# Performance work log

Hardware: AMD Instinct MI355X
Metric: run time of the kernel (lower is better)

## Reference

```python
import jax, jax.numpy as jnp
import numpy as np

N, LAT, H, R, L = 384, 64, 128, 16, 3
CUTOFF = 12.0
COORD_INIT_SCALE = 0.001


def setup_inputs() -> dict:
    key = jax.random.key(0)
    ks = jax.random.split(key, 12)
    def w(k, shape, fan):
        return jax.random.normal(k, shape, jnp.float32) / np.float32(np.sqrt(fan))
    return {
        "z": jax.random.normal(ks[0], (N, LAT), jnp.float32),
        # spread anchors so the radius graph is non-trivially sparse
        "anchor_coords": jax.random.normal(ks[1], (N, 3), jnp.float32) * 10.0,
        "proj_W": w(ks[2], (LAT, H), LAT),
        "proj_b": jnp.zeros((H,), jnp.float32),
        "eW1": w(ks[3], (L, 2 * H + R, H), 2 * H + R),
        "eb1": jnp.zeros((L, H), jnp.float32),
        "eW2": w(ks[4], (L, H, H), H),
        "eb2": jnp.zeros((L, H), jnp.float32),
        "nW1": w(ks[5], (L, 2 * H, H), 2 * H),
        "nb1": jnp.zeros((L, H), jnp.float32),
        "nW2": w(ks[6], (L, H, H), H),
        "nb2": jnp.zeros((L, H), jnp.float32),
        "cW1": w(ks[7], (L, H, H), H),
        "cb1": jnp.zeros((L, H), jnp.float32),
        # coord head scaled by coord_update_init_scale for stable coordinate updates
        "cW2": w(ks[8], (L, H, 1), H) * COORD_INIT_SCALE,
    }


def _rbf(d):
    # Gaussian radial basis expansion over [0, cutoff]
    mu = jnp.linspace(0.0, CUTOFF, R, dtype=d.dtype)            # (R,)
    gamma = jnp.asarray((R / CUTOFF) ** 2, d.dtype)
    return jnp.exp(-gamma * (d[..., None] - mu) ** 2)           # (..., R)


def reference(z, anchor_coords, proj_W, proj_b, eW1, eb1, eW2, eb2,
              nW1, nb1, nW2, nb2, cW1, cb1, cW2):
    silu = jax.nn.silu
    n = z.shape[0]
    h = z @ proj_W + proj_b                                      # (N, H)
    x = anchor_coords - anchor_coords.mean(0, keepdims=True)     # (N, 3)

    idx = jnp.arange(n)
    seq_mask = jnp.abs(idx[:, None] - idx[None, :]) == 1         # sequential edges
    eye = jnp.eye(n, dtype=bool)

    for l in range(L):
        # rebuild radius graph from current coords (dense jit-safe mask)
        diff = x[:, None, :] - x[None, :, :]                     # (N, N, 3) x_i - x_j
        d2 = jnp.sum(diff * diff, axis=-1)                       # (N, N)
        mask = ((d2 < CUTOFF ** 2) & ~eye) | seq_mask            # (N, N) bool
        maskf = mask.astype(h.dtype)
        d = jnp.sqrt(jnp.where(mask, d2, 1.0)) * maskf           # NaN-safe sqrt
        e = _rbf(d)                                              # (N, N, R)

        hi = jnp.broadcast_to(h[:, None, :], (n, n, H))          # receiver
        hj = jnp.broadcast_to(h[None, :, :], (n, n, H))          # sender
        m = silu(jnp.concatenate([hi, hj, e], -1) @ eW1[l] + eb1[l])
        m = silu(m @ eW2[l] + eb2[l]) * maskf[..., None]         # (N, N, H) messages

        agg = m.sum(1)                                           # scatter-add at receiver
        h = h + silu(jnp.concatenate([h, agg], -1) @ nW1[l] + nb1[l]) @ nW2[l] + nb2[l]

        w = (silu(m @ cW1[l] + cb1[l]) @ cW2[l]) * maskf[..., None]  # (N, N, 1)
        x = x + jnp.sum(diff * w, axis=1)                        # equivariant coord update
    return x
```

## Files before the change

kernel.cpp:

```cpp
#include <hip/hip_runtime.h>
#include <hip/hip_bf16.h>

#define NN 384
#define CUTOFF2 144.0f
#define GAMMA 1.7777778f

#define PK_L 26624
#define PK_WE 8192
#define PK_W2 10240
#define PK_C1 18432

#define STG_F32 1152
#define EDGE_SMEM ((PK_L + 8*STG_F32)*4)

#define O_XA 0
#define O_XB 4608
#define O_H 9216
#define O_A 205824
#define O_AGG 402432
#define O_HBF 599040
#define O_EREC 697344
#define O_UNITS 3056640
#define O_UCNT 3075072
#define O_MEAN 3075136
#define O_PK 3075200

typedef __bf16 bf16x8 __attribute__((ext_vector_type(8)));
typedef float f32x4 __attribute__((ext_vector_type(4)));

union ER { struct { float dx, dy, dz; unsigned j; } e; uint4 u4; };

__device__ __forceinline__ unsigned short f2bf(float f){
  unsigned u = __float_as_uint(f);
  return (unsigned short)((u + 0x7fffu + ((u >> 16) & 1u)) >> 16);
}
__device__ __forceinline__ unsigned pk2(float a, float b){
  return ((unsigned)f2bf(b) << 16) | f2bf(a);
}
__device__ __forceinline__ float silu(float x){ return x / (1.0f + __expf(-x)); }

__device__ __forceinline__ void scan_tail(
    int row, int rowsel, int t256, bool v, const float* __restrict__ x,
    uint4* __restrict__ erec, int* __restrict__ units, int* __restrict__ ucntSlot,
    int* scn){
  int* scnt  = scn + rowsel*2;
  int* sbase = scnt + 1;
  if (t256 == 0) *scnt = 0;
  __syncthreads();
  if (v) {
    float xi0 = x[row*3], xi1 = x[row*3+1], xi2 = x[row*3+2];
    for (int j = t256; j < 384; j += 256) {
      float d0 = xi0-x[j*3], d1 = xi1-x[j*3+1], d2 = xi2-x[j*3+2];
      float dd = d0*d0 + d1*d1 + d2*d2;
      bool msk = ((dd < CUTOFF2) && (j != row)) || (j == row-1) || (j == row+1);
      if (msk) {
        int ss = atomicAdd(scnt, 1);
        ER er; er.e.dx = d0; er.e.dy = d1; er.e.dz = d2; er.e.j = (unsigned)j;
        erec[row*384 + ss] = er.u4;
      }
    }
  }
  __syncthreads();
  if (v) {
    int cnt = *scnt;
    int p = (32 - (cnt & 31)) & 31;
    if (t256 < p) {
      ER er; er.e.dx = 0.f; er.e.dy = 0.f; er.e.dz = 0.f; er.e.j = (unsigned)row;
      erec[row*384 + cnt + t256] = er.u4;
    }
    if (t256 == 0) *sbase = atomicAdd(ucntSlot, (cnt + 31) >> 5);
  }
  __syncthreads();
  if (v) {
    int cnt = *scnt, nu = (cnt + 31) >> 5;
    if (t256 < nu) {
      int nv = cnt - (t256 << 5); if (nv > 32) nv = 32;
      units[*sbase + t256] = row | (t256 << 9) | (nv << 13);
    }
  }
}

__global__ __launch_bounds__(512) void k_init(
    const float* __restrict__ eW1, const float* __restrict__ eW2,
    const float* __restrict__ cW1, unsigned* __restrict__ pk,
    const float* __restrict__ anchor, const float* __restrict__ z,
    const float* __restrict__ pW, const float* __restrict__ pb,
    const float* __restrict__ eb1, float* __restrict__ h,
    unsigned short* __restrict__ hbf, float* __restrict__ A,
    float* __restrict__ agg, float* __restrict__ xB, float* __restrict__ meanw,
    uint4* __restrict__ erec, int* __restrict__ units, int* __restrict__ ucnt0){
  const int b = blockIdx.x, tid = threadIdx.x;
  if (b < 156) {
    int t = b*512 + tid;
    int layer = t / PK_L, r = t % PK_L;
    const float* src; int fr; int isWe = 0;
    if (r < PK_WE)        { fr = r;          src = eW1 + (layer*272 + 128)*128; }
    else if (r < PK_W2)   { fr = r - PK_WE;  src = eW1 + (layer*272 + 256)*128; isWe = 1; }
    else if (r < PK_C1)   { fr = r - PK_W2;  src = eW2 + layer*128*128; }
    else                  { fr = r - PK_C1;  src = cW1 + layer*128*128; }
    int tp = fr & 3, l = (fr >> 2) & 63, nc = fr >> 8;
    int n, k;
    if (!isWe) { n = nc >> 2; int c = nc & 3; k = c*32 + ((l>>4)<<3) + 2*tp; }
    else       { n = nc;                      k = ((l>>4)<<3) + 2*tp; }
    int nn = n*16 + (l & 15);
    float w0, w1;
    if (isWe) { w0 = (k < 16)   ? src[k*128+nn]     : 0.f;
                w1 = (k+1 < 16) ? src[(k+1)*128+nn] : 0.f; }
    else      { w0 = src[k*128+nn]; w1 = src[(k+1)*128+nn]; }
    pk[t] = ((unsigned)f2bf(w1) << 16) | f2bf(w0);
    return;
  }
  if (b == 156) {
    __shared__ float ssum[3];
    if (tid < 3) ssum[tid] = 0.f;
    __syncthreads();
    if (tid < 384) {
      atomicAdd(&ssum[0], anchor[tid*3]);
      atomicAdd(&ssum[1], anchor[tid*3+1]);
      atomicAdd(&ssum[2], anchor[tid*3+2]);
    }
    __syncthreads();
    if (tid < 3) meanw[tid] = ssum[tid]*(1.f/384.f);
    return;
  }
  __shared__ float sb2[2*768];
  __shared__ int scn[4];
  const int rowsel = tid >> 8, half = (tid >> 7) & 1, o = tid & 127, t256 = tid & 255;
  const int row = (b - 157)*2 + rowsel;
  float* sb = sb2 + rowsel*768;
  float* sh = sb; float* part = sb + 512; float* sz = sb + 640;

  if (half == 0) { if (o < 64) sz[o] = z[row*64 + o]; }
  else           agg[row*128 + o] = 0.f;
  if (half == 0 && o < 3) xB[row*3 + o] = anchor[row*3 + o];
  __syncthreads();
  float pp = 0.f;
  {
    int k0 = half*32;
    float p0=0,p1=0,p2=0,p3=0;
    #pragma unroll 8
    for (int k = k0; k < k0+32; k += 4) {
      p0 += sz[k]   * pW[k*128 + o];
      p1 += sz[k+1] * pW[(k+1)*128 + o];
      p2 += sz[k+2] * pW[(k+2)*128 + o];
      p3 += sz[k+3] * pW[(k+3)*128 + o];
    }
    pp = (p0+p1)+(p2+p3);
    if (half) part[o] = pp;
  }
  __syncthreads();
  if (!half) {
    float hh = pb[o] + pp + part[o];
    h[row*128 + o] = hh; sh[o] = hh;
    hbf[row*128 + o] = f2bf(hh);
  }
  __syncthreads();
  float cc = 0.f;
  {
    int k0 = half*64;
    float c0=0,c1=0,c2=0,c3=0;
    #pragma unroll 16
    for (int k = k0; k < k0+64; k += 4) {
      c0 += sh[k]   * eW1[k*128 + o];
      c1 += sh[k+1] * eW1[(k+1)*128 + o];
      c2 += sh[k+2] * eW1[(k+2)*128 + o];
      c3 += sh[k+3] * eW1[(k+3)*128 + o];
    }
    cc = (c0+c1)+(c2+c3);
    if (half) part[o] = cc;
  }
  __syncthreads();
  if (!half) A[row*128 + o] = eb1[o] + cc + part[o];

  scan_tail(row, rowsel, t256, true, anchor, erec, units, ucnt0, scn);
}

__global__ __launch_bounds__(512) void k_node(
    const float* __restrict__ nW1, const float* __restrict__ nb1,
    const float* __restrict__ nW2, const float* __restrict__ nb2,
    const float* __restrict__ eW1n, const float* __restrict__ eb1n,
    float* __restrict__ h, unsigned short* __restrict__ hbf,
    float* __restrict__ agg, float* __restrict__ A,
    const float* __restrict__ xsrc, float* __restrict__ xdst,
    const float* __restrict__ meanp,
    uint4* __restrict__ erec, int* __restrict__ units, int* __restrict__ ucntSlot){
  __shared__ float sb2[2*768];
  __shared__ int scn[4];
  const int tid = threadIdx.x;
  const int rowsel = tid >> 8, half = (tid >> 7) & 1, o = tid & 127, t256 = tid & 255;
  const int row = blockIdx.x + 256*rowsel;
  const bool v = row < NN;
  float* sb = sb2 + rowsel*768;
  float* sh = sb; float* sg = sb+128; float* st = sb+256; float* shn = sb+384; float* part = sb+512;

  if (v) {
    if (half == 0) {
      sh[o] = h[row*128 + o];
      if (o < 3) {
        float m = meanp ? meanp[o] : 0.f;
        xdst[row*3 + o] = xsrc[row*3 + o] - m;
      }
    } else {
      sg[o] = agg[row*128 + o]; agg[row*128 + o] = 0.f;
    }
  }
  __syncthreads();
  float aa = 0.f;
  if (v) {
    const float* src = half ? sg : sh;
    const float* wb  = nW1 + half*128*128;
    float a0=0,a1=0,a2=0,a3=0;
    #pragma unroll 16
    for (int k = 0; k < 128; k += 4) {
      a0 += src[k]   * wb[k*128 + o];
      a1 += src[k+1] * wb[(k+1)*128 + o];
      a2 += src[k+2] * wb[(k+2)*128 + o];
      a3 += src[k+3] * wb[(k+3)*128 + o];
    }
    aa = (a0+a1)+(a2+a3);
    if (half) part[o] = aa;
  }
  __syncthreads();
  if (v && !half) st[o] = silu(nb1[o] + aa + part[o]);
  __syncthreads();
  float bb = 0.f;
  if (v) {
    int k0 = half*64;
    float b0=0,b1=0,b2=0,b3=0;
    #pragma unroll 16
    for (int k = k0; k < k0+64; k += 4) {
      b0 += st[k]   * nW2[k*128 + o];
      b1 += st[k+1] * nW2[(k+1)*128 + o];
      b2 += st[k+2] * nW2[(k+2)*128 + o];
      b3 += st[k+3] * nW2[(k+3)*128 + o];
    }
    bb = (b0+b1)+(b2+b3);
    if (half) part[o] = bb;
  }
  __syncthreads();
  if (v && !half) {
    float hn = sh[o] + nb2[o] + bb + part[o];
    h[row*128 + o] = hn; shn[o] = hn;
    hbf[row*128 + o] = f2bf(hn);
  }
  __syncthreads();
  float cc = 0.f;
  if (v) {
    int k0 = half*64;
    float c0=0,c1=0,c2=0,c3=0;
    #pragma unroll 16
    for (int k = k0; k < k0+64; k += 4) {
      c0 += shn[k]   * eW1n[k*128 + o];
      c1 += shn[k+1] * eW1n[(k+1)*128 + o];
      c2 += shn[k+2] * eW1n[(k+2)*128 + o];
      c3 += shn[k+3] * eW1n[(k+3)*128 + o];
    }
    cc = (c0+c1)+(c2+c3);
    if (half) part[o] = cc;
  }
  __syncthreads();
  if (v && !half) A[row*128 + o] = eb1n[o] + cc + part[o];

  scan_tail(row, rowsel, t256, v, xsrc, erec, units, ucntSlot, scn);
}

#define TRANSFORM(VA, VB, FA, FB)                                              \
  _Pragma("unroll")                                                            \
  for (int c = 0; c < 4; ++c) {                                                \
    _Pragma("unroll")                                                          \
    for (int tl = 0; tl < 2; ++tl) {                                           \
      int t = 2*c + tl;                                                        \
      _Pragma("unroll")                                                        \
      for (int r = 0; r < 4; ++r) {                                            \
        stg[(quad*4 + r)*36 + tl*16 + col0] = VA[t][r];                        \
        stg[(16 + quad*4 + r)*36 + tl*16 + col0] = VB[t][r];                   \
      }                                                                        \
    }                                                                          \
    float4 lo = *(const float4*)(stg + col0*36 + quad*8);                      \
    float4 hi = *(const float4*)(stg + col0*36 + quad*8 + 4);                  \
    FA[c].u = make_uint4(pk2(lo.x,lo.y), pk2(lo.z,lo.w),                       \
                         pk2(hi.x,hi.y), pk2(hi.z,hi.w));                      \
    float4 lo2 = *(const float4*)(stg + (16 + col0)*36 + quad*8);              \
    float4 hi2 = *(const float4*)(stg + (16 + col0)*36 + quad*8 + 4);          \
    FB[c].u = make_uint4(pk2(lo2.x,lo2.y), pk2(lo2.z,lo2.w),                   \
                         pk2(hi2.x,hi2.y), pk2(hi2.z,hi2.w));                  \
  }

__global__ __launch_bounds__(512, 1) void k_edge(
    float* __restrict__ x_out, const float* __restrict__ Ag,
    const unsigned short* __restrict__ hbf, const uint4* __restrict__ erec,
    const int* __restrict__ units, const int* __restrict__ Ucnt,
    float* __restrict__ agg, const unsigned* __restrict__ pkl,
    const float* __restrict__ eb2g, const float* __restrict__ cb1g,
    const float* __restrict__ cw2g){
  extern __shared__ unsigned smem[];
  const int tid = threadIdx.x, q = tid & 63, s = tid >> 6;
  const int U = Ucnt[0];
  if (blockIdx.x >= U) return;

  for (int idx = tid; idx < PK_L/4; idx += 512)
    ((uint4*)smem)[idx] = ((const uint4*)pkl)[idx];
  __syncthreads();

  const int col0 = q & 15, quad = q >> 4;
  float eb2v[8], cb1v[8], cw2v[8];
  #pragma unroll
  for (int t = 0; t < 8; ++t) {
    int c = t*16 + col0;
    eb2v[t] = eb2g[c]; cb1v[t] = cb1g[c]; cw2v[t] = cw2g[c];
  }
  float* stg = (float*)(smem + PK_L) + s*STG_F32;
  const f32x4 z4 = {0.f, 0.f, 0.f, 0.f};
  union U8 { uint4 u; bf16x8 v; };

  for (int u = blockIdx.x + 256*s; u < U; u += 2048) {
    const int desc = units[u];
    const int i = desc & 511, b = (desc >> 9) & 15, nvalid = (desc >> 13) & 63;
    float Aval[8];
    #pragma unroll
    for (int t = 0; t < 8; ++t) Aval[t] = Ag[i*128 + t*16 + col0];
    ER e0, e1;
    e0.u4 = erec[i*384 + b*32 + col0];
    e1.u4 = erec[i*384 + b*32 + 16 + col0];
    const int j0 = (int)e0.e.j, j1 = (int)e1.e.j;
    const float d0x = e0.e.dx, d0y = e0.e.dy, d0z = e0.e.dz;
    const float d1x = e1.e.dx, d1y = e1.e.dy, d1z = e1.e.dz;
    const float dd0 = sqrtf(d0x*d0x + d0y*d0y + d0z*d0z);
    const float dd1 = sqrtf(d1x*d1x + d1y*d1y + d1z*d1z);

    U8 ha0[4], ha1[4];
    #pragma unroll
    for (int c = 0; c < 4; ++c) {
      ha0[c].u = *(const uint4*)(hbf + j0*128 + c*32 + quad*8);
      ha1[c].u = *(const uint4*)(hbf + j1*128 + c*32 + quad*8);
    }

    U8 cve0, cve1;
    if (q < 32) {
      #pragma unroll
      for (int tp = 0; tp < 4; ++tp) {
        float k0 = (float)(quad*8 + 2*tp);
        float t00 = dd0 - 0.8f*k0, t01 = dd0 - 0.8f*(k0+1.f);
        float t10 = dd1 - 0.8f*k0, t11 = dd1 - 0.8f*(k0+1.f);
        (&cve0.u.x)[tp] = pk2(__expf(-GAMMA*t00*t00), __expf(-GAMMA*t01*t01));
        (&cve1.u.x)[tp] = pk2(__expf(-GAMMA*t10*t10), __expf(-GAMMA*t11*t11));
      }
    } else { cve0.u = make_uint4(0,0,0,0); cve1.u = make_uint4(0,0,0,0); }

    f32x4 acc0[8], acc1[8];
    #pragma unroll
    for (int t = 0; t < 8; ++t) { acc0[t] = z4; acc1[t] = z4; }
    #pragma unroll
    for (int t = 0; t < 8; ++t) {
      #pragma unroll
      for (int c = 0; c < 4; ++c) {
        bf16x8 w = *(const bf16x8*)(smem + ((t*4 + c)*64 + q)*4);
        acc0[t] = __builtin_amdgcn_mfma_f32_16x16x32_bf16(ha0[c].v, w, acc0[t], 0, 0, 0);
        acc1[t] = __builtin_amdgcn_mfma_f32_16x16x32_bf16(ha1[c].v, w, acc1[t], 0, 0, 0);
      }
      bf16x8 we = *(const bf16x8*)(smem + PK_WE + (t*64 + q)*4);
      acc0[t] = __builtin_amdgcn_mfma_f32_16x16x32_bf16(cve0.v, we, acc0[t], 0, 0, 0);
      acc1[t] = __builtin_amdgcn_mfma_f32_16x16x32_bf16(cve1.v, we, acc1[t], 0, 0, 0);
    }
    #pragma unroll
    for (int t = 0; t < 8; ++t)
      #pragma unroll
      for (int r = 0; r < 4; ++r) {
        acc0[t][r] = silu(acc0[t][r] + Aval[t]);
        acc1[t][r] = silu(acc1[t][r] + Aval[t]);
      }

    U8 a20[4], a21[4];
    TRANSFORM(acc0, acc1, a20, a21);

    f32x4 m0[8], m1v[8];
    #pragma unroll
    for (int t = 0; t < 8; ++t) { m0[t] = z4; m1v[t] = z4; }
    #pragma unroll
    for (int t = 0; t < 8; ++t)
      #pragma unroll
      for (int c = 0; c < 4; ++c) {
        bf16x8 w = *(const bf16x8*)(smem + PK_W2 + ((t*4 + c)*64 + q)*4);
        m0[t] = __builtin_amdgcn_mfma_f32_16x16x32_bf16(a20[c].v, w, m0[t], 0, 0, 0);
        m1v[t] = __builtin_amdgcn_mfma_f32_16x16x32_bf16(a21[c].v, w, m1v[t], 0, 0, 0);
      }
    #pragma unroll
    for (int t = 0; t < 8; ++t) {
      float cs = 0.f;
      #pragma unroll
      for (int r = 0; r < 4; ++r) {
        m0[t][r] = silu(m0[t][r] + eb2v[t]);
        m1v[t][r] = silu(m1v[t][r] + eb2v[t]);
        if (quad*4 + r < nvalid) cs += m0[t][r];
        if (16 + quad*4 + r < nvalid) cs += m1v[t][r];
      }
      cs += __shfl_xor(cs, 16); cs += __shfl_xor(cs, 32);
      if (q < 16) atomicAdd(&agg[i*128 + t*16 + q], cs);
    }

    U8 a30[4], a31[4];
    TRANSFORM(m0, m1v, a30, a31);

    f32x4 c30[8], c31[8];
    #pragma unroll
    for (int t = 0; t < 8; ++t) { c30[t] = z4; c31[t] = z4; }
    #pragma unroll
    for (int t = 0; t < 8; ++t)
      #pragma unroll
      for (int c = 0; c < 4; ++c) {
        bf16x8 w = *(const bf16x8*)(smem + PK_C1 + ((t*4 + c)*64 + q)*4);
        c30[t] = __builtin_amdgcn_mfma_f32_16x16x32_bf16(a30[c].v, w, c30[t], 0, 0, 0);
        c31[t] = __builtin_amdgcn_mfma_f32_16x16x32_bf16(a31[c].v, w, c31[t], 0, 0, 0);
      }
    float p0[4], p1[4];
    #pragma unroll
    for (int r = 0; r < 4; ++r) {
      float pa = 0.f, pb = 0.f;
      #pragma unroll
      for (int t = 0; t < 8; ++t) {
        pa += silu(c30[t][r] + cb1v[t]) * cw2v[t];
        pb += silu(c31[t][r] + cb1v[t]) * cw2v[t];
      }
      if (quad*4 + r >= nvalid) pa = 0.f;
      if (16 + quad*4 + r >= nvalid) pb = 0.f;
      p0[r] = pa; p1[r] = pb;
    }
    #pragma unroll
    for (int r = 0; r < 4; ++r)
      #pragma unroll
      for (int off = 1; off < 16; off <<= 1) {
        p0[r] += __shfl_xor(p0[r], off);
        p1[r] += __shfl_xor(p1[r], off);
      }
    float dx0 = 0.f, dx1 = 0.f, dx2 = 0.f;
    #pragma unroll
    for (int r = 0; r < 4; ++r) {
      int el = quad*4 + r;
      float s0 = __shfl(d0x, el), s1 = __shfl(d0y, el), s2 = __shfl(d0z, el);
      if (col0 == 0) { dx0 += p0[r]*s0; dx1 += p0[r]*s1; dx2 += p0[r]*s2; }
      float u0 = __shfl(d1x, el), u1 = __shfl(d1y, el), u2 = __shfl(d1z, el);
      if (col0 == 0) { dx0 += p1[r]*u0; dx1 += p1[r]*u1; dx2 += p1[r]*u2; }
    }
    dx0 += __shfl_xor(dx0, 16); dx0 += __shfl_xor(dx0, 32);
    dx1 += __shfl_xor(dx1, 16); dx1 += __shfl_xor(dx1, 32);
    dx2 += __shfl_xor(dx2, 16); dx2 += __shfl_xor(dx2, 32);
    if (q == 0) {
      atomicAdd(&x_out[i*3 + 0], dx0);
      atomicAdd(&x_out[i*3 + 1], dx1);
      atomicAdd(&x_out[i*3 + 2], dx2);
    }
  }
}

extern "C" void kernel_launch(void* const* d_in, const int* in_sizes, int n_in,
                              void* d_out, int out_size, void* d_ws, size_t ws_size,
                              hipStream_t stream){
  const float* z      = (const float*)d_in[0];
  const float* anchor = (const float*)d_in[1];
  const float* projW  = (const float*)d_in[2];
  const float* projb  = (const float*)d_in[3];
  const float* eW1    = (const float*)d_in[4];
  const float* eb1    = (const float*)d_in[5];
  const float* eW2    = (const float*)d_in[6];
  const float* eb2    = (const float*)d_in[7];
  const float* nW1    = (const float*)d_in[8];
  const float* nb1    = (const float*)d_in[9];
  const float* nW2    = (const float*)d_in[10];
  const float* nb2    = (const float*)d_in[11];
  const float* cW1    = (const float*)d_in[12];
  const float* cb1    = (const float*)d_in[13];
  const float* cW2    = (const float*)d_in[14];
  float* out = (float*)d_out;

  char* w = (char*)d_ws;
  float* xA  = (float*)(w + O_XA);
  float* xB  = (float*)(w + O_XB);
  float* h   = (float*)(w + O_H);
  float* A   = (float*)(w + O_A);
  float* agg = (float*)(w + O_AGG);
  unsigned short* hbf = (unsigned short*)(w + O_HBF);
  uint4* erec = (uint4*)(w + O_EREC);
  int* units = (int*)(w + O_UNITS);
  int* ucnt  = (int*)(w + O_UCNT);
  float* meanw = (float*)(w + O_MEAN);
  unsigned* pk = (unsigned*)(w + O_PK);

  hipFuncSetAttribute((const void*)k_edge, hipFuncAttributeMaxDynamicSharedMemorySize, EDGE_SMEM);

  hipMemsetAsync(ucnt, 0, 12, stream);
  k_init<<<349, 512, 0, stream>>>(eW1, eW2, cW1, pk, anchor, z, projW, projb,
                                  eb1, h, hbf, A, agg, xB, meanw, erec, units, ucnt + 0);
  k_edge<<<256, 512, EDGE_SMEM, stream>>>(xB, A, hbf, erec, units, ucnt + 0,
                                          agg, pk, eb2, cb1, cW2);
  k_node<<<256, 512, 0, stream>>>(nW1, nb1, nW2, nb2, eW1 + 272*128, eb1 + 128,
                                  h, hbf, agg, A, xB, xA, (const float*)nullptr,
                                  erec, units, ucnt + 1);
  k_edge<<<256, 512, EDGE_SMEM, stream>>>(xA, A, hbf, erec, units, ucnt + 1,
                                          agg, pk + PK_L, eb2 + 128, cb1 + 128, cW2 + 128);
  k_node<<<256, 512, 0, stream>>>(nW1 + 256*128, nb1 + 128, nW2 + 128*128, nb2 + 128,
                                  eW1 + 2*272*128, eb1 + 256,
                                  h, hbf, agg, A, xA, out, meanw,
                                  erec, units, ucnt + 2);
  k_edge<<<256, 512, EDGE_SMEM, stream>>>(out, A, hbf, erec, units, ucnt + 2,
                                          agg, pk + 2*PK_L, eb2 + 256, cb1 + 256, cW2 + 256);
}
```

Measured before the change: 191.6 us.

## Fuse init, edge and node kernels into one cooperative persistent kernel

Replaces six separate launches (init, three edge passes, two node passes) with a single cooperative kernel of 256 blocks that uses grid-wide syncs between phases. Init work is redistributed: blocks 0-155 pack weights, block 0 computes the mean, and blocks 64-255 do the projection. The aim is to remove kernel launch gaps and tail effects between dependent stages. The cost is grid.sync barriers, and every block must now hold the edge-sized shared memory allocation in all phases.

```diff
diff --git a/kernel.cpp b/kernel.cpp
--- a/kernel.cpp
+++ b/kernel.cpp
@@ -1,5 +1,8 @@
 #include <hip/hip_runtime.h>
 #include <hip/hip_bf16.h>
+#include <hip/hip_cooperative_groups.h>
+
+namespace cg = cooperative_groups;
 
 #define NN 384
 #define CUTOFF2 144.0f
@@ -78,190 +81,6 @@
       units[*sbase + t256] = row | (t256 << 9) | (nv << 13);
     }
   }
-}
-
-__global__ __launch_bounds__(512) void k_init(
-    const float* __restrict__ eW1, const float* __restrict__ eW2,
-    const float* __restrict__ cW1, unsigned* __restrict__ pk,
-    const float* __restrict__ anchor, const float* __restrict__ z,
-    const float* __restrict__ pW, const float* __restrict__ pb,
-    const float* __restrict__ eb1, float* __restrict__ h,
-    unsigned short* __restrict__ hbf, float* __restrict__ A,
-    float* __restrict__ agg, float* __restrict__ xB, float* __restrict__ meanw,
-    uint4* __restrict__ erec, int* __restrict__ units, int* __restrict__ ucnt0){
-  const int b = blockIdx.x, tid = threadIdx.x;
-  if (b < 156) {
-    int t = b*512 + tid;
-    int layer = t / PK_L, r = t % PK_L;
-    const float* src; int fr; int isWe = 0;
-    if (r < PK_WE)        { fr = r;          src = eW1 + (layer*272 + 128)*128; }
-    else if (r < PK_W2)   { fr = r - PK_WE;  src = eW1 + (layer*272 + 256)*128; isWe = 1; }
-    else if (r < PK_C1)   { fr = r - PK_W2;  src = eW2 + layer*128*128; }
-    else                  { fr = r - PK_C1;  src = cW1 + layer*128*128; }
-    int tp = fr & 3, l = (fr >> 2) & 63, nc = fr >> 8;
-    int n, k;
-    if (!isWe) { n = nc >> 2; int c = nc & 3; k = c*32 + ((l>>4)<<3) + 2*tp; }
-    else       { n = nc;                      k = ((l>>4)<<3) + 2*tp; }
-    int nn = n*16 + (l & 15);
-    float w0, w1;
-    if (isWe) { w0 = (k < 16)   ? src[k*128+nn]     : 0.f;
-                w1 = (k+1 < 16) ? src[(k+1)*128+nn] : 0.f; }
-    else      { w0 = src[k*128+nn]; w1 = src[(k+1)*128+nn]; }
-    pk[t] = ((unsigned)f2bf(w1) << 16) | f2bf(w0);
-    return;
-  }
-  if (b == 156) {
-    __shared__ float ssum[3];
-    if (tid < 3) ssum[tid] = 0.f;
-    __syncthreads();
-    if (tid < 384) {
-      atomicAdd(&ssum[0], anchor[tid*3]);
-      atomicAdd(&ssum[1], anchor[tid*3+1]);
-      atomicAdd(&ssum[2], anchor[tid*3+2]);
-    }
-    __syncthreads();
-    if (tid < 3) meanw[tid] = ssum[tid]*(1.f/384.f);
-    return;
-  }
-  __shared__ float sb2[2*768];
-  __shared__ int scn[4];
-  const int rowsel = tid >> 8, half = (tid >> 7) & 1, o = tid & 127, t256 = tid & 255;
-  const int row = (b - 157)*2 + rowsel;
-  float* sb = sb2 + rowsel*768;
-  float* sh = sb; float* part = sb + 512; float* sz = sb + 640;
-
-  if (half == 0) { if (o < 64) sz[o] = z[row*64 + o]; }
-  else           agg[row*128 + o] = 0.f;
-  if (half == 0 && o < 3) xB[row*3 + o] = anchor[row*3 + o];
-  __syncthreads();
-  float pp = 0.f;
-  {
-    int k0 = half*32;
-    float p0=0,p1=0,p2=0,p3=0;
-    #pragma unroll 8
-    for (int k = k0; k < k0+32; k += 4) {
-      p0 += sz[k]   * pW[k*128 + o];
-      p1 += sz[k+1] * pW[(k+1)*128 + o];
-      p2 += sz[k+2] * pW[(k+2)*128 + o];
-      p3 += sz[k+3] * pW[(k+3)*128 + o];
-    }
-    pp = (p0+p1)+(p2+p3);
-    if (half) part[o] = pp;
-  }
-  __syncthreads();
-  if (!half) {
-    float hh = pb[o] + pp + part[o];
-    h[row*128 + o] = hh; sh[o] = hh;
-    hbf[row*128 + o] = f2bf(hh);
-  }
-  __syncthreads();
-  float cc = 0.f;
-  {
-    int k0 = half*64;
-    float c0=0,c1=0,c2=0,c3=0;
-    #pragma unroll 16
-    for (int k = k0; k < k0+64; k += 4) {
-      c0 += sh[k]   * eW1[k*128 + o];
-      c1 += sh[k+1] * eW1[(k+1)*128 + o];
-      c2 += sh[k+2] * eW1[(k+2)*128 + o];
-      c3 += sh[k+3] * eW1[(k+3)*128 + o];
-    }
-    cc = (c0+c1)+(c2+c3);
-    if (half) part[o] = cc;
-  }
-  __syncthreads();
-  if (!half) A[row*128 + o] = eb1[o] + cc + part[o];
-
-  scan_tail(row, rowsel, t256, true, anchor, erec, units, ucnt0, scn);
-}
-
-__global__ __launch_bounds__(512) void k_node(
-    const float* __restrict__ nW1, const float* __restrict__ nb1,
-    const float* __restrict__ nW2, const float* __restrict__ nb2,
-    const float* __restrict__ eW1n, const float* __restrict__ eb1n,
-    float* __restrict__ h, unsigned short* __restrict__ hbf,
-    float* __restrict__ agg, float* __restrict__ A,
-    const float* __restrict__ xsrc, float* __restrict__ xdst,
-    const float* __restrict__ meanp,
-    uint4* __restrict__ erec, int* __restrict__ units, int* __restrict__ ucntSlot){
-  __shared__ float sb2[2*768];
-  __shared__ int scn[4];
-  const int tid = threadIdx.x;
-  const int rowsel = tid >> 8, half = (tid >> 7) & 1, o = tid & 127, t256 = tid & 255;
-  const int row = blockIdx.x + 256*rowsel;
-  const bool v = row < NN;
-  float* sb = sb2 + rowsel*768;
-  float* sh = sb; float* sg = sb+128; float* st = sb+256; float* shn = sb+384; float* part = sb+512;
-
-  if (v) {
-    if (half == 0) {
-      sh[o] = h[row*128 + o];
-      if (o < 3) {
-        float m = meanp ? meanp[o] : 0.f;
-        xdst[row*3 + o] = xsrc[row*3 + o] - m;
-      }
-    } else {
-      sg[o] = agg[row*128 + o]; agg[row*128 + o] = 0.f;
-    }
-  }
-  __syncthreads();
-  float aa = 0.f;
-  if (v) {
-    const float* src = half ? sg : sh;
-    const float* wb  = nW1 + half*128*128;
-    float a0=0,a1=0,a2=0,a3=0;
-    #pragma unroll 16
-    for (int k = 0; k < 128; k += 4) {
-      a0 += src[k]   * wb[k*128 + o];
-      a1 += src[k+1] * wb[(k+1)*128 + o];
-      a2 += src[k+2] * wb[(k+2)*128 + o];
-      a3 += src[k+3] * wb[(k+3)*128 + o];
-    }
-    aa = (a0+a1)+(a2+a3);
-    if (half) part[o] = aa;
-  }
-  __syncthreads();
-  if (v && !half) st[o] = silu(nb1[o] + aa + part[o]);
-  __syncthreads();
-  float bb = 0.f;
-  if (v) {
-    int k0 = half*64;
-    float b0=0,b1=0,b2=0,b3=0;
-    #pragma unroll 16
-    for (int k = k0; k < k0+64; k += 4) {
-      b0 += st[k]   * nW2[k*128 + o];
-      b1 += st[k+1] * nW2[(k+1)*128 + o];
-      b2 += st[k+2] * nW2[(k+2)*128 + o];
-      b3 += st[k+3] * nW2[(k+3)*128 + o];
-    }
-    bb = (b0+b1)+(b2+b3);
-    if (half) part[o] = bb;
-  }
-  __syncthreads();
-  if (v && !half) {
-    float hn = sh[o] + nb2[o] + bb + part[o];
-    h[row*128 + o] = hn; shn[o] = hn;
-    hbf[row*128 + o] = f2bf(hn);
-  }
-  __syncthreads();
-  float cc = 0.f;
-  if (v) {
-    int k0 = half*64;
-    float c0=0,c1=0,c2=0,c3=0;
-    #pragma unroll 16
-    for (int k = k0; k < k0+64; k += 4) {
-      c0 += shn[k]   * eW1n[k*128 + o];
-      c1 += shn[k+1] * eW1n[(k+1)*128 + o];
-      c2 += shn[k+2] * eW1n[(k+2)*128 + o];
-      c3 += shn[k+3] * eW1n[(k+3)*128 + o];
-    }
-    cc = (c0+c1)+(c2+c3);
-    if (half) part[o] = cc;
-  }
-  __syncthreads();
-  if (v && !half) A[row*128 + o] = eb1n[o] + cc + part[o];
-
-  scan_tail(row, rowsel, t256, v, xsrc, erec, units, ucntSlot, scn);
 }
 
 #define TRANSFORM(VA, VB, FA, FB)                                              \
@@ -286,22 +105,14 @@
                          pk2(hi2.x,hi2.y), pk2(hi2.z,hi2.w));                  \
   }
 
-__global__ __launch_bounds__(512, 1) void k_edge(
+__device__ __forceinline__ void edge_phase(
     float* __restrict__ x_out, const float* __restrict__ Ag,
     const unsigned short* __restrict__ hbf, const uint4* __restrict__ erec,
-    const int* __restrict__ units, const int* __restrict__ Ucnt,
-    float* __restrict__ agg, const unsigned* __restrict__ pkl,
+    const int* __restrict__ units, const int U,
+    float* __restrict__ agg, unsigned* smem,
     const float* __restrict__ eb2g, const float* __restrict__ cb1g,
     const float* __restrict__ cw2g){
-  extern __shared__ unsigned smem[];
   const int tid = threadIdx.x, q = tid & 63, s = tid >> 6;
-  const int U = Ucnt[0];
-  if (blockIdx.x >= U) return;
-
-  for (int idx = tid; idx < PK_L/4; idx += 512)
-    ((uint4*)smem)[idx] = ((const uint4*)pkl)[idx];
-  __syncthreads();
-
   const int col0 = q & 15, quad = q >> 4;
   float eb2v[8], cb1v[8], cw2v[8];
   #pragma unroll
@@ -449,6 +260,217 @@
       atomicAdd(&x_out[i*3 + 1], dx1);
       atomicAdd(&x_out[i*3 + 2], dx2);
     }
+  }
+}
+
+__device__ __forceinline__ void node_phase(
+    const float* __restrict__ nW1l, const float* __restrict__ nb1l,
+    const float* __restrict__ nW2l, const float* __restrict__ nb2l,
+    const float* __restrict__ eW1n, const float* __restrict__ eb1n,
+    float* __restrict__ h, unsigned short* __restrict__ hbf,
+    float* __restrict__ agg, float* __restrict__ A,
+    const float* __restrict__ xsrc, float* __restrict__ xdst,
+    const float* __restrict__ meanp,
+    uint4* __restrict__ erec, int* __restrict__ units, int* __restrict__ ucntSlot,
+    float* sb2f, int* scn){
+  const int tid = threadIdx.x;
+  const int rowsel = tid >> 8, half = (tid >> 7) & 1, o = tid & 127, t256 = tid & 255;
+  const int row = blockIdx.x + 256*rowsel;
+  const bool v = row < NN;
+  float* sb = sb2f + rowsel*768;
+  float* sh = sb; float* sg = sb+128; float* st = sb+256; float* shn = sb+384; float* part = sb+512;
+
+  if (v) {
+    if (half == 0) {
+      sh[o] = h[row*128 + o];
+      if (o < 3) {
+        float m = meanp ? meanp[o] : 0.f;
+        xdst[row*3 + o] = xsrc[row*3 + o] - m;
+      }
+    } else {
+      sg[o] = agg[row*128 + o]; agg[row*128 + o] = 0.f;
+    }
+  }
+  __syncthreads();
+  float aa = 0.f;
+  if (v) {
+    const float* src = half ? sg : sh;
+    const float* wb  = nW1l + half*128*128;
+    float a0=0,a1=0,a2=0,a3=0;
+    #pragma unroll 16
+    for (int k = 0; k < 128; k += 4) {
+      a0 += src[k]   * wb[k*128 + o];
+      a1 += src[k+1] * wb[(k+1)*128 + o];
+      a2 += src[k+2] * wb[(k+2)*128 + o];
+      a3 += src[k+3] * wb[(k+3)*128 + o];
+    }
+    aa = (a0+a1)+(a2+a3);
+    if (half) part[o] = aa;
+  }
+  __syncthreads();
+  if (v && !half) st[o] = silu(nb1l[o] + aa + part[o]);
+  __syncthreads();
+  float bb = 0.f;
+  if (v) {
+    int k0 = half*64;
+    float b0=0,b1=0,b2=0,b3=0;
+    #pragma unroll 16
+    for (int k = k0; k < k0+64; k += 4) {
+      b0 += st[k]   * nW2l[k*128 + o];
+      b1 += st[k+1] * nW2l[(k+1)*128 + o];
+      b2 += st[k+2] * nW2l[(k+2)*128 + o];
+      b3 += st[k+3] * nW2l[(k+3)*128 + o];
+    }
+    bb = (b0+b1)+(b2+b3);
+    if (half) part[o] = bb;
+  }
+  __syncthreads();
+  if (v && !half) {
+    float hn = sh[o] + nb2l[o] + bb + part[o];
+    h[row*128 + o] = hn; shn[o] = hn;
+    hbf[row*128 + o] = f2bf(hn);
+  }
+  __syncthreads();
+  float cc = 0.f;
+  if (v) {
+    int k0 = half*64;
+    float c0=0,c1=0,c2=0,c3=0;
+    #pragma unroll 16
+    for (int k = k0; k < k0+64; k += 4) {
+      c0 += shn[k]   * eW1n[k*128 + o];
+      c1 += shn[k+1] * eW1n[(k+1)*128 + o];
+      c2 += shn[k+2] * eW1n[(k+2)*128 + o];
+      c3 += shn[k+3] * eW1n[(k+3)*128 + o];
+    }
+    cc = (c0+c1)+(c2+c3);
+    if (half) part[o] = cc;
+  }
+  __syncthreads();
+  if (v && !half) A[row*128 + o] = eb1n[o] + cc + part[o];
+
+  scan_tail(row, rowsel, t256, v, xsrc, erec, units, ucntSlot, scn);
+}
+
+__global__ __launch_bounds__(512, 1) void k_fused(
+    const float* __restrict__ z, const float* __restrict__ anchor,
+    const float* __restrict__ projW, const float* __restrict__ projb,
+    const float* __restrict__ eW1, const float* __restrict__ eb1,
+    const float* __restrict__ eW2, const float* __restrict__ eb2,
+    const float* __restrict__ nW1, const float* __restrict__ nb1,
+    const float* __restrict__ nW2, const float* __restrict__ nb2,
+    const float* __restrict__ cW1, const float* __restrict__ cb1,
+    const float* __restrict__ cW2,
+    float* __restrict__ out,
+    float* __restrict__ xA, float* __restrict__ xB,
+    float* __restrict__ h, unsigned short* __restrict__ hbf,
+    float* __restrict__ A, float* __restrict__ agg,
+    uint4* __restrict__ erec, int* __restrict__ units, int* __restrict__ ucnt,
+    float* __restrict__ meanw, unsigned* __restrict__ pk){
+  cg::grid_group grid = cg::this_grid();
+  extern __shared__ unsigned smem[];
+  const int b = blockIdx.x, tid = threadIdx.x;
+  const int rowsel = tid >> 8, half = (tid >> 7) & 1, o = tid & 127, t256 = tid & 255;
+  float* sb2f = (float*)(smem + PK_L);
+  int* scn = (int*)(sb2f + 1536);
+
+  {
+    int t = b*512 + tid;
+    if (t < 3*PK_L) {
+      int layer = t / PK_L, r = t % PK_L;
+      const float* src; int fr; int isWe = 0;
+      if (r < PK_WE)        { fr = r;          src = eW1 + (layer*272 + 128)*128; }
+      else if (r < PK_W2)   { fr = r - PK_WE;  src = eW1 + (layer*272 + 256)*128; isWe = 1; }
+      else if (r < PK_C1)   { fr = r - PK_W2;  src = eW2 + layer*128*128; }
+      else                  { fr = r - PK_C1;  src = cW1 + layer*128*128; }
+      int tp = fr & 3, ll = (fr >> 2) & 63, nc = fr >> 8;
+      int n, k;
+      if (!isWe) { n = nc >> 2; int c = nc & 3; k = c*32 + ((ll>>4)<<3) + 2*tp; }
+      else       { n = nc;                      k = ((ll>>4)<<3) + 2*tp; }
+      int nn2 = n*16 + (ll & 15);
+      float w0, w1;
+      if (isWe) { w0 = (k < 16)   ? src[k*128+nn2]     : 0.f;
+                  w1 = (k+1 < 16) ? src[(k+1)*128+nn2] : 0.f; }
+      else      { w0 = src[k*128+nn2]; w1 = src[(k+1)*128+nn2]; }
+      pk[t] = ((unsigned)f2bf(w1) << 16) | f2bf(w0);
+    }
+  }
+  if (b == 0) {
+    float* ssum = sb2f;
+    if (tid < 3) ssum[tid] = 0.f;
+    __syncthreads();
+    if (tid < 384) {
+      atomicAdd(&ssum[0], anchor[tid*3]);
+      atomicAdd(&ssum[1], anchor[tid*3+1]);
+      atomicAdd(&ssum[2], anchor[tid*3+2]);
+    }
+    __syncthreads();
+    if (tid < 3) meanw[tid] = ssum[tid]*(1.f/384.f);
+  }
+  if (b >= 64) {
+    const int row = (b - 64)*2 + rowsel;
+    float* sb = sb2f + rowsel*768;
+    float* sh = sb; float* part = sb + 512; float* sz = sb + 640;
+    if (half == 0) { if (o < 64) sz[o] = z[row*64 + o]; }
+    else           agg[row*128 + o] = 0.f;
+    if (half == 0 && o < 3) xB[row*3 + o] = anchor[row*3 + o];
+    __syncthreads();
+    float pp = 0.f;
+    {
+      int k0 = half*32;
+      float p0=0,p1=0,p2=0,p3=0;
+      #pragma unroll 8
+      for (int k = k0; k < k0+32; k += 4) {
+        p0 += sz[k]   * projW[k*128 + o];
+        p1 += sz[k+1] * projW[(k+1)*128 + o];
+        p2 += sz[k+2] * projW[(k+2)*128 + o];
+        p3 += sz[k+3] * projW[(k+3)*128 + o];
+      }
+      pp = (p0+p1)+(p2+p3);
+      if (half) part[o] = pp;
+    }
+    __syncthreads();
+    if (!half) {
+      float hh = projb[o] + pp + part[o];
+      h[row*128 + o] = hh; sh[o] = hh;
+      hbf[row*128 + o] = f2bf(hh);
+    }
+    __syncthreads();
+    float cc = 0.f;
+    {
+      int k0 = half*64;
+      float c0=0,c1=0,c2=0,c3=0;
+      #pragma unroll 16
+      for (int k = k0; k < k0+64; k += 4) {
+        c0 += sh[k]   * eW1[k*128 + o];
+        c1 += sh[k+1] * eW1[(k+1)*128 + o];
+        c2 += sh[k+2] * eW1[(k+2)*128 + o];
+        c3 += sh[k+3] * eW1[(k+3)*128 + o];
+      }
+      cc = (c0+c1)+(c2+c3);
+      if (half) part[o] = cc;
+    }
+    __syncthreads();
+    if (!half) A[row*128 + o] = eb1[o] + cc + part[o];
+  }
+  scan_tail(b*2 + rowsel, rowsel, t256, b < 192, anchor, erec, units, ucnt, scn);
+
+  for (int l = 0; l < 3; ++l) {
+    grid.sync();
+    for (int idx = tid; idx < PK_L/4; idx += 512)
+      ((uint4*)smem)[idx] = ((const uint4*)(pk + l*PK_L))[idx];
+    __syncthreads();
+    const int U = ((volatile const int*)ucnt)[l];
+    float* x_out = (l == 0) ? xB : ((l == 1) ? xA : out);
+    edge_phase(x_out, A, hbf, erec, units, U, agg, smem,
+               eb2 + l*128, cb1 + l*128, cW2 + l*128);
+    if (l == 2) break;
+    grid.sync();
+    node_phase(nW1 + l*256*128, nb1 + l*128, nW2 + l*128*128, nb2 + l*128,
+               eW1 + (l+1)*272*128, eb1 + (l+1)*128,
+               h, hbf, agg, A,
+               (l == 0) ? xB : xA, (l == 0) ? xA : out,
+               (l == 0) ? (const float*)nullptr : meanw,
+               erec, units, ucnt + (l+1), sb2f, scn);
   }
 }
 
@@ -485,22 +507,12 @@
   float* meanw = (float*)(w + O_MEAN);
   unsigned* pk = (unsigned*)(w + O_PK);
 
-  hipFuncSetAttribute((const void*)k_edge, hipFuncAttributeMaxDynamicSharedMemorySize, EDGE_SMEM);
+  hipFuncSetAttribute((const void*)k_fused, hipFuncAttributeMaxDynamicSharedMemorySize, EDGE_SMEM);
 
   hipMemsetAsync(ucnt, 0, 12, stream);
-  k_init<<<349, 512, 0, stream>>>(eW1, eW2, cW1, pk, anchor, z, projW, projb,
-                                  eb1, h, hbf, A, agg, xB, meanw, erec, units, ucnt + 0);
-  k_edge<<<256, 512, EDGE_SMEM, stream>>>(xB, A, hbf, erec, units, ucnt + 0,
-                                          agg, pk, eb2, cb1, cW2);
-  k_node<<<256, 512, 0, stream>>>(nW1, nb1, nW2, nb2, eW1 + 272*128, eb1 + 128,
-                                  h, hbf, agg, A, xB, xA, (const float*)nullptr,
-                                  erec, units, ucnt + 1);
-  k_edge<<<256, 512, EDGE_SMEM, stream>>>(xA, A, hbf, erec, units, ucnt + 1,
-                                          agg, pk + PK_L, eb2 + 128, cb1 + 128, cW2 + 128);
-  k_node<<<256, 512, 0, stream>>>(nW1 + 256*128, nb1 + 128, nW2 + 128*128, nb2 + 128,
-                                  eW1 + 2*272*128, eb1 + 256,
-                                  h, hbf, agg, A, xA, out, meanw,
-                                  erec, units, ucnt + 2);
-  k_edge<<<256, 512, EDGE_SMEM, stream>>>(out, A, hbf, erec, units, ucnt + 2,
-                                          agg, pk + 2*PK_L, eb2 + 256, cb1 + 256, cW2 + 256);
-}
+  void* args[] = { &z, &anchor, &projW, &projb, &eW1, &eb1, &eW2, &eb2,
+                   &nW1, &nb1, &nW2, &nb2, &cW1, &cb1, &cW2, &out,
+                   &xA, &xB, &h, &hbf, &A, &agg, &erec, &units, &ucnt, &meanw, &pk };
+  hipLaunchCooperativeKernel((const void*)k_fused, dim3(256), dim3(512),
+                             args, EDGE_SMEM, stream);
+}
```

Measured after the change: 326.8 us. 1.71x slower.
